# Optimization experiments

Measured on AMD Instinct MI355X. Metric: run time of the kernel, lower is better.

The kernel has to match this reference:

```python
import jax, jax.numpy as jnp
import numpy as np

B, S, E, H = 4, 2048, 1024, 16
D = E // H  # head_dim = 64


def setup_inputs() -> dict:
    key = jax.random.key(0)
    ks = jax.random.split(key, 5)
    return {
        "x": jax.random.normal(ks[0], (B, S, E), dtype=jnp.float32),
        "w_qkv": jax.random.normal(ks[1], (3 * E, E), dtype=jnp.float32) * (E ** -0.5),
        "b_qkv": jax.random.normal(ks[2], (3 * E,), dtype=jnp.float32) * 0.02,
        "w_proj": jax.random.normal(ks[3], (E, E), dtype=jnp.float32) * (E ** -0.5),
        "b_proj": jax.random.normal(ks[4], (E,), dtype=jnp.float32) * 0.02,
    }


def reference(x, w_qkv, b_qkv, w_proj, b_proj):
    # fused QKV projection: [B,S,E] -> [B,S,3E] -> [B,S,3,H,D]
    qkv = (jnp.einsum("bse,fe->bsf", x, w_qkv) + b_qkv).reshape(B, S, 3, H, D)
    q, k, v = qkv[:, :, 0], qkv[:, :, 1], qkv[:, :, 2]  # each [B,S,H,D]
    scale = 1.0 / jnp.sqrt(jnp.asarray(D, dtype=q.dtype))
    scores = jnp.einsum("bqhd,bkhd->bhqk", q, k) * scale  # [B,H,S,S]
    attn = jax.nn.softmax(scores, axis=-1)
    out = jnp.einsum("bhqk,bkhd->bqhd", attn, v).reshape(B, S, E)
    return jnp.einsum("bse,fe->bsf", out, w_proj) + b_proj
```

## Files before the change

kernel.cpp:

```cpp
#include <hip/hip_runtime.h>
#include <cstdint>
#include <cstddef>

#define B_ 4
#define S_ 2048
#define E_ 1024
#define H_ 16
#define D_ 64
#define M_ (B_*S_)
#define NE_ ((size_t)B_*H_*S_*D_)

typedef unsigned int  u32;
typedef unsigned short u16;
typedef __attribute__((ext_vector_type(8))) short bf16x8;
typedef __attribute__((ext_vector_type(4))) float f32x4;
typedef __attribute__((ext_vector_type(2))) unsigned int u32x2;

__device__ __forceinline__ u16 f2bf(float x) {
    u32 u = __float_as_uint(x);
    u32 r = (u + 0x7FFFu + ((u >> 16) & 1u)) >> 16;
    return (u16)r;
}
__device__ __forceinline__ float bf2f(u16 h) { return __uint_as_float((u32)h << 16); }

__device__ __forceinline__ u32 cvtpk_bf16(float lo, float hi) {
    u32 r;
    asm("v_cvt_pk_bf16_f32 %0, %1, %2" : "=v"(r) : "v"(lo), "v"(hi));
    return r;
}

__device__ __forceinline__ void gload_lds16(const void* gsrc, void* lds) {
    __builtin_amdgcn_global_load_lds(
        (const __attribute__((address_space(1))) u32*)gsrc,
        (__attribute__((address_space(3))) u32*)lds, 16, 0, 0);
}


__global__ __launch_bounds__(256)
void convert_img(const float* __restrict__ src, u16* __restrict__ dh, u16* __restrict__ dl)
{
    const int tile = blockIdx.x;
    const int rt = tile >> 5, kt = tile & 31;
    const size_t tb = (size_t)tile * 2048;
    const int ci = threadIdx.x;
    const int l  = ci >> 3;
    const int ph = ci & 7;
    const int s  = ph ^ (l & 7);
    const int r  = (l << 1) | (s >> 2);
    const int k0 = (s & 3) << 3;
    const float* sp = src + ((size_t)(rt * 64 + r)) * 1024 + kt * 32 + k0;
    const float4 f0 = *(const float4*)sp;
    const float4 f1 = *(const float4*)(sp + 4);
    const float vals[8] = {f0.x, f0.y, f0.z, f0.w, f1.x, f1.y, f1.z, f1.w};
    __align__(16) short hs[8];
    __align__(16) short ls[8];
    #pragma unroll
    for (int j = 0; j < 8; ++j) {
        const u16 h = f2bf(vals[j]);
        hs[j] = (short)h;
        ls[j] = (short)f2bf(vals[j] - bf2f(h));
    }
    *(bf16x8*)(dh + tb + ci * 8) = *(const bf16x8*)hs;
    *(bf16x8*)(dl + tb + ci * 8) = *(const bf16x8*)ls;
}

__global__ __launch_bounds__(256, 2)
void gemm_qkv(const u16* __restrict__ AIh, const u16* __restrict__ AIl,
              const u16* __restrict__ BIh, const u16* __restrict__ BIl,
              const float* __restrict__ bias,
              u16* __restrict__ qh, u16* __restrict__ ql,
              u16* __restrict__ kh,
              u16* __restrict__ vh, u16* __restrict__ vl)
{
    __shared__ __align__(16) u16 sT[2][8][2048];

    const int tid = threadIdx.x, lane = tid & 63, w = tid >> 6;
    const int quad = lane >> 4, l15 = lane & 15;
    const int bx = blockIdx.x, by = blockIdx.y;
    const int m0  = bx * 128;
    const int n0  = by * 128;
    const int mt0 = bx * 2;
    const int nt0 = by * 2;
    const int rw  = w >> 1;
    const int cw  = w & 1;

    const u16* srcq[8];
    #pragma unroll
    for (int it = 0; it < 8; ++it) {
        const int g = w * 8 + it;
        const int t = g >> 2, qtr = g & 3;
        const u16* img = (t < 2) ? AIh : (t < 4) ? AIl : (t < 6) ? BIh : BIl;
        const int rtile = ((t < 4) ? mt0 : nt0) + (t & 1);
        srcq[it] = img + (size_t)rtile * (32 * 2048) + qtr * 512 + lane * 8;
    }

    f32x4 acc[4][4];
    #pragma unroll
    for (int i = 0; i < 4; ++i)
        #pragma unroll
        for (int j = 0; j < 4; ++j)
            acc[i][j] = (f32x4){0.f, 0.f, 0.f, 0.f};

    #pragma unroll
    for (int it = 0; it < 8; ++it)
        gload_lds16(srcq[it], (char*)&sT[0][0][0] + (w * 8 + it) * 1024);
    __syncthreads();

    #pragma unroll 2
    for (int kt = 0; kt < 32; ++kt) {
        const int cur = kt & 1;
        if (kt < 31) {
            #pragma unroll
            for (int it = 0; it < 8; ++it)
                gload_lds16(srcq[it] + (size_t)(kt + 1) * 2048,
                            (char*)&sT[cur ^ 1][0][0] + (w * 8 + it) * 1024);
        }
        bf16x8 aH[4], aL[4], bH[4], bL[4];
        #pragma unroll
        for (int i = 0; i < 4; ++i) {
            const int r = i * 16 + l15, l = r >> 1;
            const int off = l * 64 + (((((r & 1) << 2) + quad) ^ (l & 7)) << 3);
            aH[i] = *(const bf16x8*)&sT[cur][rw][off];
            aL[i] = *(const bf16x8*)&sT[cur][2 + rw][off];
        }
        #pragma unroll
        for (int j = 0; j < 4; ++j) {
            const int r = j * 16 + l15, l = r >> 1;
            const int off = l * 64 + (((((r & 1) << 2) + quad) ^ (l & 7)) << 3);
            bH[j] = *(const bf16x8*)&sT[cur][4 + cw][off];
            bL[j] = *(const bf16x8*)&sT[cur][6 + cw][off];
        }
        __builtin_amdgcn_s_setprio(1);
        #pragma unroll
        for (int i = 0; i < 4; ++i)
            #pragma unroll
            for (int j = 0; j < 4; ++j) {
                acc[i][j] = __builtin_amdgcn_mfma_f32_16x16x32_bf16(aL[i], bH[j], acc[i][j], 0, 0, 0);
                acc[i][j] = __builtin_amdgcn_mfma_f32_16x16x32_bf16(aH[i], bL[j], acc[i][j], 0, 0, 0);
                acc[i][j] = __builtin_amdgcn_mfma_f32_16x16x32_bf16(aH[i], bH[j], acc[i][j], 0, 0, 0);
            }
        __builtin_amdgcn_s_setprio(0);
        __syncthreads();
    }

    const int fbase = n0 + cw * 64;
    float bj[4];
    #pragma unroll
    for (int j = 0; j < 4; ++j) bj[j] = bias[fbase + j * 16 + l15];

    const int cR = fbase >> 10;
    const int hh = (fbase >> 6) & 15;
    #pragma unroll
    for (int i = 0; i < 4; ++i)
        #pragma unroll
        for (int j = 0; j < 4; ++j)
            #pragma unroll
            for (int reg = 0; reg < 4; ++reg) {
                float val = acc[i][j][reg] + bj[j];
                const int m = m0 + rw * 64 + i * 16 + quad * 4 + reg;
                const int d = j * 16 + l15;
                const int bb = m >> 11, s = m & 2047;
                const int bh = bb * 16 + hh;
                if (cR == 0) val *= 0.18033688011112042f;
                const u16 h = f2bf(val);
                if (cR == 0) {
                    const u16 lo = f2bf(val - bf2f(h));
                    const size_t idx = ((size_t)bh * 2048 + s) * 64 + d;
                    qh[idx] = h; ql[idx] = lo;
                } else if (cR == 1) {
                    const size_t tile = (size_t)bh * 32 + (s >> 6);
                    const int r = s & 63;
                    const size_t off = (tile << 12) + r * 64 + (((d >> 3) ^ (r & 7)) << 3) + (d & 7);
                    kh[off] = h;
                } else {
                    const u16 lo = f2bf(val - bf2f(h));
                    const size_t tile = (size_t)bh * 32 + (s >> 6);
                    const size_t off = (tile << 12) + d * 64 + ((((s & 63) >> 3) ^ (d & 7)) << 3) + (s & 7);
                    vh[off] = h; vl[off] = lo;
                }
            }
}

__global__ __launch_bounds__(512, 2)
void gemm_proj(const u16* __restrict__ AIh, const u16* __restrict__ AIl,
               const u16* __restrict__ BIh, const u16* __restrict__ BIl,
               const float* __restrict__ bias, float* __restrict__ Cout)
{
    __shared__ __align__(16) u16 sT[2][12][2048];

    const int tid = threadIdx.x, lane = tid & 63, w = tid >> 6;
    const int quad = lane >> 4, l15 = lane & 15;
    const int bx = blockIdx.x, by = blockIdx.y;
    const int m0  = bx * 256;
    const int n0  = by * 128;
    const int mt0 = bx * 4;
    const int nt0 = by * 2;
    const int rw  = w >> 1;
    const int cw  = w & 1;

    const u16* srcq[6];
    #pragma unroll
    for (int it = 0; it < 6; ++it) {
        const int g = w * 6 + it;
        const int t = g >> 2, qtr = g & 3;
        const u16* img = (t < 4) ? AIh : (t < 8) ? AIl : (t < 10) ? BIh : BIl;
        const int rtile = (t < 8) ? (mt0 + (t & 3)) : (nt0 + (t & 1));
        srcq[it] = img + (size_t)rtile * (32 * 2048) + qtr * 512 + lane * 8;
    }

    f32x4 acc[4][4];
    #pragma unroll
    for (int i = 0; i < 4; ++i)
        #pragma unroll
        for (int j = 0; j < 4; ++j)
            acc[i][j] = (f32x4){0.f, 0.f, 0.f, 0.f};

    #pragma unroll
    for (int it = 0; it < 6; ++it)
        gload_lds16(srcq[it], (char*)&sT[0][0][0] + (w * 6 + it) * 1024);
    __syncthreads();

    #pragma unroll 2
    for (int kt = 0; kt < 32; ++kt) {
        const int cur = kt & 1;
        bf16x8 aH[4], aL[4], bH[4], bL[4];
        #pragma unroll
        for (int i = 0; i < 4; ++i) {
            const int r = i * 16 + l15, l = r >> 1;
            const int off = l * 64 + (((((r & 1) << 2) + quad) ^ (l & 7)) << 3);
            aH[i] = *(const bf16x8*)&sT[cur][rw][off];
            aL[i] = *(const bf16x8*)&sT[cur][4 + rw][off];
        }
        #pragma unroll
        for (int j = 0; j < 4; ++j) {
            const int r = j * 16 + l15, l = r >> 1;
            const int off = l * 64 + (((((r & 1) << 2) + quad) ^ (l & 7)) << 3);
            bH[j] = *(const bf16x8*)&sT[cur][8 + cw][off];
            bL[j] = *(const bf16x8*)&sT[cur][10 + cw][off];
        }
        if (kt < 31) {
            #pragma unroll
            for (int it = 0; it < 6; ++it)
                gload_lds16(srcq[it] + (size_t)(kt + 1) * 2048,
                            (char*)&sT[cur ^ 1][0][0] + (w * 6 + it) * 1024);
        }
        __builtin_amdgcn_s_setprio(1);
        #pragma unroll
        for (int i = 0; i < 4; ++i)
            #pragma unroll
            for (int j = 0; j < 4; ++j) {
                acc[i][j] = __builtin_amdgcn_mfma_f32_16x16x32_bf16(aL[i], bH[j], acc[i][j], 0, 0, 0);
                acc[i][j] = __builtin_amdgcn_mfma_f32_16x16x32_bf16(aH[i], bL[j], acc[i][j], 0, 0, 0);
                acc[i][j] = __builtin_amdgcn_mfma_f32_16x16x32_bf16(aH[i], bH[j], acc[i][j], 0, 0, 0);
            }
        __builtin_amdgcn_s_setprio(0);
        __syncthreads();
    }

    const int fbase = n0 + cw * 64;
    float bj[4];
    #pragma unroll
    for (int j = 0; j < 4; ++j) bj[j] = bias[fbase + j * 16 + l15];
    #pragma unroll
    for (int i = 0; i < 4; ++i)
        #pragma unroll
        for (int j = 0; j < 4; ++j)
            #pragma unroll
            for (int reg = 0; reg < 4; ++reg) {
                const int m = m0 + rw * 64 + i * 16 + quad * 4 + reg;
                const int f = fbase + j * 16 + l15;
                Cout[(size_t)m * 1024 + f] = acc[i][j][reg] + bj[j];
            }
}

__global__ __launch_bounds__(256, 3)
void attn_mfma(const u16* __restrict__ qh, const u16* __restrict__ ql,
               const u16* __restrict__ kh,
               const u16* __restrict__ vh, const u16* __restrict__ vl,
               u16* __restrict__ oh, u16* __restrict__ ol)
{
    __shared__ __align__(16) u16 KV[3][4096];

    const int tid  = threadIdx.x;
    const int lane = tid & 63, w = tid >> 6;
    const int quad = lane >> 4, l15 = lane & 15;
    const int bh = blockIdx.y;
    const int q0 = blockIdx.x * 128 + w * 32;

    bf16x8 Qf[2][2][2];
    #pragma unroll
    for (int qs = 0; qs < 2; ++qs)
        #pragma unroll
        for (int kk = 0; kk < 2; ++kk) {
            const size_t idx = ((size_t)bh * S_ + q0 + qs * 16 + l15) * 64 + kk * 32 + quad * 8;
            Qf[qs][kk][0] = *(const bf16x8*)(qh + idx);
            Qf[qs][kk][1] = *(const bf16x8*)(ql + idx);
        }

    f32x4 O[2][4];
    float l_part[2] = {0.f, 0.f};
    #pragma unroll
    for (int qs = 0; qs < 2; ++qs)
        #pragma unroll
        for (int ds = 0; ds < 4; ++ds)
            O[qs][ds] = (f32x4){0.f, 0.f, 0.f, 0.f};

    const char* gk[3] = {(const char*)kh, (const char*)vh, (const char*)vl};

    for (int kt = 0; kt < S_ / 64; ++kt) {
        __syncthreads();
        const size_t tb = (((size_t)bh * 32 + kt) << 13);
        #pragma unroll
        for (int a = 0; a < 3; ++a)
            #pragma unroll
            for (int it = 0; it < 2; ++it) {
                const int off = w * 2048 + it * 1024;
                gload_lds16(gk[a] + tb + off + lane * 16, (char*)&KV[a][0] + off);
            }
        __syncthreads();

        f32x4 S[2][4];
        #pragma unroll
        for (int qs = 0; qs < 2; ++qs)
            #pragma unroll
            for (int ks = 0; ks < 4; ++ks)
                S[qs][ks] = (f32x4){-23.083120654223414f, -23.083120654223414f,
                                    -23.083120654223414f, -23.083120654223414f};

        __builtin_amdgcn_s_setprio(1);
        #pragma unroll
        for (int ks = 0; ks < 4; ++ks) {
            const int r = ks * 16 + l15;
            #pragma unroll
            for (int kk = 0; kk < 2; ++kk) {
                const int c = (kk * 4 + quad) ^ (r & 7);
                const bf16x8 Kh = *(const bf16x8*)&KV[0][r * 64 + c * 8];
                #pragma unroll
                for (int qs = 0; qs < 2; ++qs) {
                    S[qs][ks] = __builtin_amdgcn_mfma_f32_16x16x32_bf16(Kh, Qf[qs][kk][1], S[qs][ks], 0, 0, 0);
                    S[qs][ks] = __builtin_amdgcn_mfma_f32_16x16x32_bf16(Kh, Qf[qs][kk][0], S[qs][ks], 0, 0, 0);
                }
            }
        }
        __builtin_amdgcn_s_setprio(0);

        u32 PA[2][2][4];
        #pragma unroll
        for (int qs = 0; qs < 2; ++qs) {
            float lsum = 0.f;
            u32 PK[4][2];
            #pragma unroll
            for (int ks = 0; ks < 4; ++ks) {
                const float p0 = __builtin_exp2f(S[qs][ks][0]);
                const float p1 = __builtin_exp2f(S[qs][ks][1]);
                const float p2 = __builtin_exp2f(S[qs][ks][2]);
                const float p3 = __builtin_exp2f(S[qs][ks][3]);
                lsum += (p0 + p1) + (p2 + p3);
                PK[ks][0] = cvtpk_bf16(p0, p1);
                PK[ks][1] = cvtpk_bf16(p2, p3);
            }
            l_part[qs] += lsum;
            #pragma unroll
            for (int kk = 0; kk < 2; ++kk) {
                const u32x2 t0 = __builtin_amdgcn_permlane32_swap(PK[2 * kk][0], PK[2 * kk + 1][0], false, false);
                const u32x2 w02 = __builtin_amdgcn_permlane16_swap(t0.x, t0.y, false, false);
                const u32x2 t1 = __builtin_amdgcn_permlane32_swap(PK[2 * kk][1], PK[2 * kk + 1][1], false, false);
                const u32x2 w13 = __builtin_amdgcn_permlane16_swap(t1.x, t1.y, false, false);
                PA[qs][kk][0] = w02.x;
                PA[qs][kk][1] = w13.x;
                PA[qs][kk][2] = w02.y;
                PA[qs][kk][3] = w13.y;
            }
        }

        __builtin_amdgcn_s_setprio(1);
        #pragma unroll
        for (int kk = 0; kk < 2; ++kk) {
            union { u32 w4[4]; bf16x8 v; } pu0, pu1;
            #pragma unroll
            for (int c = 0; c < 4; ++c) { pu0.w4[c] = PA[0][kk][c]; pu1.w4[c] = PA[1][kk][c]; }
            const bf16x8 paf[2] = {pu0.v, pu1.v};
            #pragma unroll
            for (int ds = 0; ds < 4; ++ds) {
                const int r = ds * 16 + l15;
                const int c = (kk * 4 + quad) ^ (r & 7);
                const bf16x8 Vh = *(const bf16x8*)&KV[1][r * 64 + c * 8];
                const bf16x8 Vl = *(const bf16x8*)&KV[2][r * 64 + c * 8];
                #pragma unroll
                for (int qs = 0; qs < 2; ++qs) {
                    O[qs][ds] = __builtin_amdgcn_mfma_f32_16x16x32_bf16(Vl, paf[qs], O[qs][ds], 0, 0, 0);
                    O[qs][ds] = __builtin_amdgcn_mfma_f32_16x16x32_bf16(Vh, paf[qs], O[qs][ds], 0, 0, 0);
                }
            }
        }
        __builtin_amdgcn_s_setprio(0);
    }

    float linv[2];
    #pragma unroll
    for (int qs = 0; qs < 2; ++qs) {
        float rs = l_part[qs];
        rs += __shfl_xor(rs, 16);
        rs += __shfl_xor(rs, 32);
        linv[qs] = 1.f / rs;
    }

    const int bb = bh >> 4, hh = bh & 15;
    #pragma unroll
    for (int qs = 0; qs < 2; ++qs) {
        const float inv = linv[qs];
        const int s = q0 + qs * 16 + l15;
        const int m = bb * 2048 + s;
        const int mt = m >> 6, r = m & 63;
        const int l = r >> 1;
        const size_t tb0 = ((size_t)(mt * 32 + hh * 2)) * 2048;
        #pragma unroll
        for (int ds = 0; ds < 4; ++ds) {
            const int d0 = ds * 16 + quad * 4;
            const float v0 = O[qs][ds][0] * inv;
            const float v1 = O[qs][ds][1] * inv;
            const float v2 = O[qs][ds][2] * inv;
            const float v3 = O[qs][ds][3] * inv;
            const u32 h01 = cvtpk_bf16(v0, v1);
            const u32 h23 = cvtpk_bf16(v2, v3);
            const float r0 = v0 - bf2f((u16)h01);
            const float r1 = v1 - bf2f((u16)(h01 >> 16));
            const float r2 = v2 - bf2f((u16)h23);
            const float r3 = v3 - bf2f((u16)(h23 >> 16));
            const u32 l01 = cvtpk_bf16(r0, r1);
            const u32 l23 = cvtpk_bf16(r2, r3);
            const int c  = (d0 & 31) >> 3;
            const int ph = (((r & 1) << 2) + c) ^ (l & 7);
            const size_t off = tb0 + (size_t)(d0 >> 5) * 2048 + l * 64 + ph * 8 + (d0 & 7);
            *(u32x2*)(oh + off) = (u32x2){h01, h23};
            *(u32x2*)(ol + off) = (u32x2){l01, l23};
        }
    }
}

extern "C" void kernel_launch(void* const* d_in, const int* in_sizes, int n_in,
                              void* d_out, int out_size, void* d_ws, size_t ws_size,
                              hipStream_t stream) {
    const float* x      = (const float*)d_in[0];
    const float* w_qkv  = (const float*)d_in[1];
    const float* b_qkv  = (const float*)d_in[2];
    const float* w_proj = (const float*)d_in[3];
    const float* b_proj = (const float*)d_in[4];
    float* out = (float*)d_out;

    u16* qh  = (u16*)d_ws;
    u16* ql  = qh + NE_;
    u16* kh  = ql + NE_;
    u16* vh  = kh + NE_;
    u16* vl  = vh + NE_;
    u16* xh  = vl + NE_;
    u16* xl  = xh + NE_;
    u16* wqh = xl + NE_;
    u16* wql = wqh + (size_t)3 * 1024 * 1024;
    u16* oh  = xh;
    u16* ol  = xl;
    u16* wph = wqh;
    u16* wpl = wph + (size_t)1024 * 1024;

    convert_img<<<128 * 32, 256, 0, stream>>>(x, xh, xl);
    convert_img<<<48 * 32, 256, 0, stream>>>(w_qkv, wqh, wql);

    {
        dim3 grid(M_ / 128, (3 * E_) / 128);
        gemm_qkv<<<grid, 256, 0, stream>>>(xh, xl, wqh, wql,
                                           b_qkv, qh, ql, kh, vh, vl);
    }
    {
        dim3 grid(S_ / 128, B_ * H_);
        attn_mfma<<<grid, 256, 0, stream>>>(qh, ql, kh, vh, vl, oh, ol);
    }
    convert_img<<<16 * 32, 256, 0, stream>>>(w_proj, wph, wpl);
    {
        dim3 grid(M_ / 256, E_ / 128);
        gemm_proj<<<grid, 512, 0, stream>>>(oh, ol, wph, wpl, b_proj, out);
    }
}
```

Baseline: 427.8 us.

## Double-buffer attention K/V tiles, remap attention grid, shrink proj GEMM tiles

The attention kernel now double-buffers its K/V LDS tiles, prefetching the next tile before computing on the current one, so there is one barrier per iteration instead of two. It also launches a flat grid and remaps block indices so that consecutive blocks are spread across heads, which may change L2 locality or balance across XCDs. The projection GEMM drops from 256x128 tiles with 512 threads to 128x128 tiles with 256 threads, doubling the block count, and issues its prefetch before the LDS reads. These changes double the attention LDS footprint, which could reduce occupancy, and the GEMM now reloads each B tile for twice as many blocks.

```diff
diff --git a/kernel.cpp b/kernel.cpp
--- a/kernel.cpp
+++ b/kernel.cpp
@@ -181,30 +181,30 @@
             }
 }
 
-__global__ __launch_bounds__(512, 2)
+__global__ __launch_bounds__(256, 2)
 void gemm_proj(const u16* __restrict__ AIh, const u16* __restrict__ AIl,
                const u16* __restrict__ BIh, const u16* __restrict__ BIl,
                const float* __restrict__ bias, float* __restrict__ Cout)
 {
-    __shared__ __align__(16) u16 sT[2][12][2048];
+    __shared__ __align__(16) u16 sT[2][8][2048];
 
     const int tid = threadIdx.x, lane = tid & 63, w = tid >> 6;
     const int quad = lane >> 4, l15 = lane & 15;
     const int bx = blockIdx.x, by = blockIdx.y;
-    const int m0  = bx * 256;
+    const int m0  = bx * 128;
     const int n0  = by * 128;
-    const int mt0 = bx * 4;
+    const int mt0 = bx * 2;
     const int nt0 = by * 2;
     const int rw  = w >> 1;
     const int cw  = w & 1;
 
-    const u16* srcq[6];
-    #pragma unroll
-    for (int it = 0; it < 6; ++it) {
-        const int g = w * 6 + it;
+    const u16* srcq[8];
+    #pragma unroll
+    for (int it = 0; it < 8; ++it) {
+        const int g = w * 8 + it;
         const int t = g >> 2, qtr = g & 3;
-        const u16* img = (t < 4) ? AIh : (t < 8) ? AIl : (t < 10) ? BIh : BIl;
-        const int rtile = (t < 8) ? (mt0 + (t & 3)) : (nt0 + (t & 1));
+        const u16* img = (t < 2) ? AIh : (t < 4) ? AIl : (t < 6) ? BIh : BIl;
+        const int rtile = ((t < 4) ? mt0 : nt0) + (t & 1);
         srcq[it] = img + (size_t)rtile * (32 * 2048) + qtr * 512 + lane * 8;
     }
 
@@ -216,33 +216,33 @@
             acc[i][j] = (f32x4){0.f, 0.f, 0.f, 0.f};
 
     #pragma unroll
-    for (int it = 0; it < 6; ++it)
-        gload_lds16(srcq[it], (char*)&sT[0][0][0] + (w * 6 + it) * 1024);
+    for (int it = 0; it < 8; ++it)
+        gload_lds16(srcq[it], (char*)&sT[0][0][0] + (w * 8 + it) * 1024);
     __syncthreads();
 
     #pragma unroll 2
     for (int kt = 0; kt < 32; ++kt) {
         const int cur = kt & 1;
+        if (kt < 31) {
+            #pragma unroll
+            for (int it = 0; it < 8; ++it)
+                gload_lds16(srcq[it] + (size_t)(kt + 1) * 2048,
+                            (char*)&sT[cur ^ 1][0][0] + (w * 8 + it) * 1024);
+        }
         bf16x8 aH[4], aL[4], bH[4], bL[4];
         #pragma unroll
         for (int i = 0; i < 4; ++i) {
             const int r = i * 16 + l15, l = r >> 1;
             const int off = l * 64 + (((((r & 1) << 2) + quad) ^ (l & 7)) << 3);
             aH[i] = *(const bf16x8*)&sT[cur][rw][off];
-            aL[i] = *(const bf16x8*)&sT[cur][4 + rw][off];
+            aL[i] = *(const bf16x8*)&sT[cur][2 + rw][off];
         }
         #pragma unroll
         for (int j = 0; j < 4; ++j) {
             const int r = j * 16 + l15, l = r >> 1;
             const int off = l * 64 + (((((r & 1) << 2) + quad) ^ (l & 7)) << 3);
-            bH[j] = *(const bf16x8*)&sT[cur][8 + cw][off];
-            bL[j] = *(const bf16x8*)&sT[cur][10 + cw][off];
-        }
-        if (kt < 31) {
-            #pragma unroll
-            for (int it = 0; it < 6; ++it)
-                gload_lds16(srcq[it] + (size_t)(kt + 1) * 2048,
-                            (char*)&sT[cur ^ 1][0][0] + (w * 6 + it) * 1024);
+            bH[j] = *(const bf16x8*)&sT[cur][4 + cw][off];
+            bL[j] = *(const bf16x8*)&sT[cur][6 + cw][off];
         }
         __builtin_amdgcn_s_setprio(1);
         #pragma unroll
@@ -279,13 +279,16 @@
                const u16* __restrict__ vh, const u16* __restrict__ vl,
                u16* __restrict__ oh, u16* __restrict__ ol)
 {
-    __shared__ __align__(16) u16 KV[3][4096];
+    __shared__ __align__(16) u16 KV[2][3][4096];
 
     const int tid  = threadIdx.x;
     const int lane = tid & 63, w = tid >> 6;
     const int quad = lane >> 4, l15 = lane & 15;
-    const int bh = blockIdx.y;
-    const int q0 = blockIdx.x * 128 + w * 32;
+
+    const int flat = blockIdx.x;
+    const int logical = (flat & 7) * 128 + (flat >> 3);
+    const int bh = logical >> 4;
+    const int q0 = (logical & 15) * 128 + w * 32;
 
     bf16x8 Qf[2][2][2];
     #pragma unroll
@@ -307,17 +310,32 @@
 
     const char* gk[3] = {(const char*)kh, (const char*)vh, (const char*)vl};
 
-    for (int kt = 0; kt < S_ / 64; ++kt) {
-        __syncthreads();
-        const size_t tb = (((size_t)bh * 32 + kt) << 13);
+    {
+        const size_t tb = ((size_t)bh * 32) << 13;
         #pragma unroll
         for (int a = 0; a < 3; ++a)
             #pragma unroll
             for (int it = 0; it < 2; ++it) {
                 const int off = w * 2048 + it * 1024;
-                gload_lds16(gk[a] + tb + off + lane * 16, (char*)&KV[a][0] + off);
-            }
-        __syncthreads();
+                gload_lds16(gk[a] + tb + off + lane * 16, (char*)&KV[0][a][0] + off);
+            }
+    }
+    __syncthreads();
+
+    for (int kt = 0; kt < S_ / 64; ++kt) {
+        const int cur = kt & 1;
+
+        if (kt < S_ / 64 - 1) {
+            const size_t tb = (((size_t)bh * 32 + kt + 1) << 13);
+            #pragma unroll
+            for (int a = 0; a < 3; ++a)
+                #pragma unroll
+                for (int it = 0; it < 2; ++it) {
+                    const int off = w * 2048 + it * 1024;
+                    gload_lds16(gk[a] + tb + off + lane * 16,
+                                (char*)&KV[cur ^ 1][a][0] + off);
+                }
+        }
 
         f32x4 S[2][4];
         #pragma unroll
@@ -334,7 +352,7 @@
             #pragma unroll
             for (int kk = 0; kk < 2; ++kk) {
                 const int c = (kk * 4 + quad) ^ (r & 7);
-                const bf16x8 Kh = *(const bf16x8*)&KV[0][r * 64 + c * 8];
+                const bf16x8 Kh = *(const bf16x8*)&KV[cur][0][r * 64 + c * 8];
                 #pragma unroll
                 for (int qs = 0; qs < 2; ++qs) {
                     S[qs][ks] = __builtin_amdgcn_mfma_f32_16x16x32_bf16(Kh, Qf[qs][kk][1], S[qs][ks], 0, 0, 0);
@@ -384,8 +402,8 @@
             for (int ds = 0; ds < 4; ++ds) {
                 const int r = ds * 16 + l15;
                 const int c = (kk * 4 + quad) ^ (r & 7);
-                const bf16x8 Vh = *(const bf16x8*)&KV[1][r * 64 + c * 8];
-                const bf16x8 Vl = *(const bf16x8*)&KV[2][r * 64 + c * 8];
+                const bf16x8 Vh = *(const bf16x8*)&KV[cur][1][r * 64 + c * 8];
+                const bf16x8 Vl = *(const bf16x8*)&KV[cur][2][r * 64 + c * 8];
                 #pragma unroll
                 for (int qs = 0; qs < 2; ++qs) {
                     O[qs][ds] = __builtin_amdgcn_mfma_f32_16x16x32_bf16(Vl, paf[qs], O[qs][ds], 0, 0, 0);
@@ -394,6 +412,8 @@
             }
         }
         __builtin_amdgcn_s_setprio(0);
+
+        __syncthreads();
     }
 
     float linv[2];
@@ -471,12 +491,11 @@
                                            b_qkv, qh, ql, kh, vh, vl);
     }
     {
-        dim3 grid(S_ / 128, B_ * H_);
-        attn_mfma<<<grid, 256, 0, stream>>>(qh, ql, kh, vh, vl, oh, ol);
+        attn_mfma<<<1024, 256, 0, stream>>>(qh, ql, kh, vh, vl, oh, ol);
     }
     convert_img<<<16 * 32, 256, 0, stream>>>(w_proj, wph, wpl);
     {
-        dim3 grid(M_ / 256, E_ / 128);
-        gemm_proj<<<grid, 512, 0, stream>>>(oh, ol, wph, wpl, b_proj, out);
-    }
-}
+        dim3 grid(M_ / 128, E_ / 128);
+        gemm_proj<<<grid, 256, 0, stream>>>(oh, ol, wph, wpl, b_proj, out);
+    }
+}
```

After: 432.0 us. Within noise of the previous version (+1.0%).

## Double-buffer attention K/V tiles, remap blocks to XCDs, merge input conversions

Applied to the files above, without the earlier changes.

The attention kernel now holds two LDS buffers for the K/V tiles and prefetches the next tile with async global-to-LDS loads while the current one is being computed. This drops one barrier per iteration and hides load latency. The grid is flattened and remapped so that consecutive blocks on the same XCD share a (batch, head) and reuse K/V in L2. The two fp32-to-bf16 split conversions for x and w_qkv are merged into a single launch. Doubling LDS to 48KB per block may reduce occupancy below the 3 blocks per CU requested in the launch bounds, and the prefetch only has a barrier at the end of each iteration, which relies on the load-to-LDS ordering being correct.

```diff
diff --git a/kernel.cpp b/kernel.cpp
--- a/kernel.cpp
+++ b/kernel.cpp
@@ -35,6 +35,38 @@
         (__attribute__((address_space(3))) u32*)lds, 16, 0, 0);
 }
 
+
+__global__ __launch_bounds__(256)
+void convert_img2(const float* __restrict__ s1, u16* __restrict__ dh1, u16* __restrict__ dl1, int n1,
+                  const float* __restrict__ s2, u16* __restrict__ dh2, u16* __restrict__ dl2)
+{
+    int tile = blockIdx.x;
+    const float* src; u16* dh; u16* dl;
+    if (tile < n1) { src = s1; dh = dh1; dl = dl1; }
+    else           { tile -= n1; src = s2; dh = dh2; dl = dl2; }
+    const int rt = tile >> 5, kt = tile & 31;
+    const size_t tb = (size_t)tile * 2048;
+    const int ci = threadIdx.x;
+    const int l  = ci >> 3;
+    const int ph = ci & 7;
+    const int s  = ph ^ (l & 7);
+    const int r  = (l << 1) | (s >> 2);
+    const int k0 = (s & 3) << 3;
+    const float* sp = src + ((size_t)(rt * 64 + r)) * 1024 + kt * 32 + k0;
+    const float4 f0 = *(const float4*)sp;
+    const float4 f1 = *(const float4*)(sp + 4);
+    const float vals[8] = {f0.x, f0.y, f0.z, f0.w, f1.x, f1.y, f1.z, f1.w};
+    __align__(16) short hs[8];
+    __align__(16) short ls[8];
+    #pragma unroll
+    for (int j = 0; j < 8; ++j) {
+        const u16 h = f2bf(vals[j]);
+        hs[j] = (short)h;
+        ls[j] = (short)f2bf(vals[j] - bf2f(h));
+    }
+    *(bf16x8*)(dh + tb + ci * 8) = *(const bf16x8*)hs;
+    *(bf16x8*)(dl + tb + ci * 8) = *(const bf16x8*)ls;
+}
 
 __global__ __launch_bounds__(256)
 void convert_img(const float* __restrict__ src, u16* __restrict__ dh, u16* __restrict__ dl)
@@ -279,13 +311,16 @@
                const u16* __restrict__ vh, const u16* __restrict__ vl,
                u16* __restrict__ oh, u16* __restrict__ ol)
 {
-    __shared__ __align__(16) u16 KV[3][4096];
+    __shared__ __align__(16) u16 KV[2][3][4096];
 
     const int tid  = threadIdx.x;
     const int lane = tid & 63, w = tid >> 6;
     const int quad = lane >> 4, l15 = lane & 15;
-    const int bh = blockIdx.y;
-    const int q0 = blockIdx.x * 128 + w * 32;
+
+    const int flat = blockIdx.x;
+    const int logical = (flat & 7) * 128 + (flat >> 3);
+    const int bh = logical >> 4;
+    const int q0 = (logical & 15) * 128 + w * 32;
 
     bf16x8 Qf[2][2][2];
     #pragma unroll
@@ -307,17 +342,32 @@
 
     const char* gk[3] = {(const char*)kh, (const char*)vh, (const char*)vl};
 
-    for (int kt = 0; kt < S_ / 64; ++kt) {
-        __syncthreads();
-        const size_t tb = (((size_t)bh * 32 + kt) << 13);
+    {
+        const size_t tb = ((size_t)bh * 32) << 13;
         #pragma unroll
         for (int a = 0; a < 3; ++a)
             #pragma unroll
             for (int it = 0; it < 2; ++it) {
                 const int off = w * 2048 + it * 1024;
-                gload_lds16(gk[a] + tb + off + lane * 16, (char*)&KV[a][0] + off);
-            }
-        __syncthreads();
+                gload_lds16(gk[a] + tb + off + lane * 16, (char*)&KV[0][a][0] + off);
+            }
+    }
+    __syncthreads();
+
+    for (int kt = 0; kt < S_ / 64; ++kt) {
+        const int cur = kt & 1;
+
+        if (kt < S_ / 64 - 1) {
+            const size_t tb = (((size_t)bh * 32 + kt + 1) << 13);
+            #pragma unroll
+            for (int a = 0; a < 3; ++a)
+                #pragma unroll
+                for (int it = 0; it < 2; ++it) {
+                    const int off = w * 2048 + it * 1024;
+                    gload_lds16(gk[a] + tb + off + lane * 16,
+                                (char*)&KV[cur ^ 1][a][0] + off);
+                }
+        }
 
         f32x4 S[2][4];
         #pragma unroll
@@ -334,7 +384,7 @@
             #pragma unroll
             for (int kk = 0; kk < 2; ++kk) {
                 const int c = (kk * 4 + quad) ^ (r & 7);
-                const bf16x8 Kh = *(const bf16x8*)&KV[0][r * 64 + c * 8];
+                const bf16x8 Kh = *(const bf16x8*)&KV[cur][0][r * 64 + c * 8];
                 #pragma unroll
                 for (int qs = 0; qs < 2; ++qs) {
                     S[qs][ks] = __builtin_amdgcn_mfma_f32_16x16x32_bf16(Kh, Qf[qs][kk][1], S[qs][ks], 0, 0, 0);
@@ -384,8 +434,8 @@
             for (int ds = 0; ds < 4; ++ds) {
                 const int r = ds * 16 + l15;
                 const int c = (kk * 4 + quad) ^ (r & 7);
-                const bf16x8 Vh = *(const bf16x8*)&KV[1][r * 64 + c * 8];
-                const bf16x8 Vl = *(const bf16x8*)&KV[2][r * 64 + c * 8];
+                const bf16x8 Vh = *(const bf16x8*)&KV[cur][1][r * 64 + c * 8];
+                const bf16x8 Vl = *(const bf16x8*)&KV[cur][2][r * 64 + c * 8];
                 #pragma unroll
                 for (int qs = 0; qs < 2; ++qs) {
                     O[qs][ds] = __builtin_amdgcn_mfma_f32_16x16x32_bf16(Vl, paf[qs], O[qs][ds], 0, 0, 0);
@@ -394,6 +444,8 @@
             }
         }
         __builtin_amdgcn_s_setprio(0);
+
+        __syncthreads();
     }
 
     float linv[2];
@@ -462,8 +514,8 @@
     u16* wph = wqh;
     u16* wpl = wph + (size_t)1024 * 1024;
 
-    convert_img<<<128 * 32, 256, 0, stream>>>(x, xh, xl);
-    convert_img<<<48 * 32, 256, 0, stream>>>(w_qkv, wqh, wql);
+    convert_img2<<<128 * 32 + 48 * 32, 256, 0, stream>>>(
+        x, xh, xl, 128 * 32, w_qkv, wqh, wql);
 
     {
         dim3 grid(M_ / 128, (3 * E_) / 128);
@@ -471,8 +523,7 @@
                                            b_qkv, qh, ql, kh, vh, vl);
     }
     {
-        dim3 grid(S_ / 128, B_ * H_);
-        attn_mfma<<<grid, 256, 0, stream>>>(qh, ql, kh, vh, vl, oh, ol);
+        attn_mfma<<<1024, 256, 0, stream>>>(qh, ql, kh, vh, vl, oh, ol);
     }
     convert_img<<<16 * 32, 256, 0, stream>>>(w_proj, wph, wpl);
     {
```

Measured after the change: 413.5 us. -3.3%, faster.

## Double-buffer K/V tiles in attention, widen blocks, and merge conversion launches

Applied to the files above, without the earlier changes.

The attention kernel now uses 512-thread blocks covering 256 queries. It double-buffers the K/V LDS tiles, prefetching the next tile while computing the current one, which leaves one barrier per iteration instead of two. Block indices are remapped so that blocks from the same head land together, for better L2 reuse of K/V. The three fp32-to-bf16 split conversion launches are merged into one kernel, with w_proj getting its own workspace slot, which removes two launches. In exchange LDS use doubles and fewer waves may be resident.

```diff
diff --git a/kernel.cpp b/kernel.cpp
--- a/kernel.cpp
+++ b/kernel.cpp
@@ -37,9 +37,15 @@
 
 
 __global__ __launch_bounds__(256)
-void convert_img(const float* __restrict__ src, u16* __restrict__ dh, u16* __restrict__ dl)
+void convert_img3(const float* __restrict__ s1, u16* __restrict__ dh1, u16* __restrict__ dl1, int n1,
+                  const float* __restrict__ s2, u16* __restrict__ dh2, u16* __restrict__ dl2, int n2,
+                  const float* __restrict__ s3, u16* __restrict__ dh3, u16* __restrict__ dl3)
 {
-    const int tile = blockIdx.x;
+    int tile = blockIdx.x;
+    const float* src; u16* dh; u16* dl;
+    if (tile < n1)           { src = s1; dh = dh1; dl = dl1; }
+    else if (tile < n1 + n2) { tile -= n1; src = s2; dh = dh2; dl = dl2; }
+    else                     { tile -= n1 + n2; src = s3; dh = dh3; dl = dl3; }
     const int rt = tile >> 5, kt = tile & 31;
     const size_t tb = (size_t)tile * 2048;
     const int ci = threadIdx.x;
@@ -273,19 +279,22 @@
             }
 }
 
-__global__ __launch_bounds__(256, 3)
+__global__ __launch_bounds__(512, 4)
 void attn_mfma(const u16* __restrict__ qh, const u16* __restrict__ ql,
                const u16* __restrict__ kh,
                const u16* __restrict__ vh, const u16* __restrict__ vl,
                u16* __restrict__ oh, u16* __restrict__ ol)
 {
-    __shared__ __align__(16) u16 KV[3][4096];
+    __shared__ __align__(16) u16 KV[2][3][4096];
 
     const int tid  = threadIdx.x;
     const int lane = tid & 63, w = tid >> 6;
     const int quad = lane >> 4, l15 = lane & 15;
-    const int bh = blockIdx.y;
-    const int q0 = blockIdx.x * 128 + w * 32;
+
+    const int flat = blockIdx.x;
+    const int logical = (flat & 7) * 64 + (flat >> 3);
+    const int bh = logical >> 3;
+    const int q0 = (logical & 7) * 256 + w * 32;
 
     bf16x8 Qf[2][2][2];
     #pragma unroll
@@ -307,17 +316,28 @@
 
     const char* gk[3] = {(const char*)kh, (const char*)vh, (const char*)vl};
 
+    {
+        const size_t tb = ((size_t)bh * 32) << 13;
+        #pragma unroll
+        for (int a = 0; a < 3; ++a) {
+            const int off = w * 1024;
+            gload_lds16(gk[a] + tb + off + lane * 16, (char*)&KV[0][a][0] + off);
+        }
+    }
+    __syncthreads();
+
     for (int kt = 0; kt < S_ / 64; ++kt) {
-        __syncthreads();
-        const size_t tb = (((size_t)bh * 32 + kt) << 13);
-        #pragma unroll
-        for (int a = 0; a < 3; ++a)
-            #pragma unroll
-            for (int it = 0; it < 2; ++it) {
-                const int off = w * 2048 + it * 1024;
-                gload_lds16(gk[a] + tb + off + lane * 16, (char*)&KV[a][0] + off);
-            }
-        __syncthreads();
+        const int cur = kt & 1;
+
+        if (kt < S_ / 64 - 1) {
+            const size_t tb = (((size_t)bh * 32 + kt + 1) << 13);
+            #pragma unroll
+            for (int a = 0; a < 3; ++a) {
+                const int off = w * 1024;
+                gload_lds16(gk[a] + tb + off + lane * 16,
+                            (char*)&KV[cur ^ 1][a][0] + off);
+            }
+        }
 
         f32x4 S[2][4];
         #pragma unroll
@@ -334,7 +354,7 @@
             #pragma unroll
             for (int kk = 0; kk < 2; ++kk) {
                 const int c = (kk * 4 + quad) ^ (r & 7);
-                const bf16x8 Kh = *(const bf16x8*)&KV[0][r * 64 + c * 8];
+                const bf16x8 Kh = *(const bf16x8*)&KV[cur][0][r * 64 + c * 8];
                 #pragma unroll
                 for (int qs = 0; qs < 2; ++qs) {
                     S[qs][ks] = __builtin_amdgcn_mfma_f32_16x16x32_bf16(Kh, Qf[qs][kk][1], S[qs][ks], 0, 0, 0);
@@ -384,8 +404,8 @@
             for (int ds = 0; ds < 4; ++ds) {
                 const int r = ds * 16 + l15;
                 const int c = (kk * 4 + quad) ^ (r & 7);
-                const bf16x8 Vh = *(const bf16x8*)&KV[1][r * 64 + c * 8];
-                const bf16x8 Vl = *(const bf16x8*)&KV[2][r * 64 + c * 8];
+                const bf16x8 Vh = *(const bf16x8*)&KV[cur][1][r * 64 + c * 8];
+                const bf16x8 Vl = *(const bf16x8*)&KV[cur][2][r * 64 + c * 8];
                 #pragma unroll
                 for (int qs = 0; qs < 2; ++qs) {
                     O[qs][ds] = __builtin_amdgcn_mfma_f32_16x16x32_bf16(Vl, paf[qs], O[qs][ds], 0, 0, 0);
@@ -394,6 +414,8 @@
             }
         }
         __builtin_amdgcn_s_setprio(0);
+
+        __syncthreads();
     }
 
     float linv[2];
@@ -457,13 +479,15 @@
     u16* xl  = xh + NE_;
     u16* wqh = xl + NE_;
     u16* wql = wqh + (size_t)3 * 1024 * 1024;
+    u16* wph = wql + (size_t)3 * 1024 * 1024;
+    u16* wpl = wph + (size_t)1024 * 1024;
     u16* oh  = xh;
     u16* ol  = xl;
-    u16* wph = wqh;
-    u16* wpl = wph + (size_t)1024 * 1024;
-
-    convert_img<<<128 * 32, 256, 0, stream>>>(x, xh, xl);
-    convert_img<<<48 * 32, 256, 0, stream>>>(w_qkv, wqh, wql);
+
+    convert_img3<<<128 * 32 + 48 * 32 + 16 * 32, 256, 0, stream>>>(
+        x, xh, xl, 128 * 32,
+        w_qkv, wqh, wql, 48 * 32,
+        w_proj, wph, wpl);
 
     {
         dim3 grid(M_ / 128, (3 * E_) / 128);
@@ -471,10 +495,8 @@
                                            b_qkv, qh, ql, kh, vh, vl);
     }
     {
-        dim3 grid(S_ / 128, B_ * H_);
-        attn_mfma<<<grid, 256, 0, stream>>>(qh, ql, kh, vh, vl, oh, ol);
-    }
-    convert_img<<<16 * 32, 256, 0, stream>>>(w_proj, wph, wpl);
+        attn_mfma<<<512, 512, 0, stream>>>(qh, ql, kh, vh, vl, oh, ol);
+    }
     {
         dim3 grid(M_ / 256, E_ / 128);
         gemm_proj<<<grid, 512, 0, stream>>>(oh, ol, wph, wpl, b_proj, out);
```

New measurement: 464.1 us. 8.5% more time.
